# Kernel optimization log

Measured on AMD Instinct MI355X. Metric: run time of the kernel, lower is better.

The kernel has to match this reference:

```python
import jax, jax.numpy as jnp
import numpy as np

N_NODES = 4096
N_EDGES = 131072
IN_DIM = 40
HID = 128
OUT = 128
GAT_H = 2
GAT_C = 64
D_MODEL = 128
N_HEAD = 4
FF_DIM = 2048
N_LAYERS = 2
EPS = 1e-5
NEG_SLOPE = 0.2


def _layer_norm(x, g, b):
    mu = x.mean(-1, keepdims=True)
    var = ((x - mu) ** 2).mean(-1, keepdims=True)
    return (x - mu) / jnp.sqrt(var + EPS) * g + b


def _gat_conv(h, src, dst, W, a_src, a_dst, bias):
    # PyG GATConv, concat=True, eval mode (no dropout). Self loops already in (src, dst).
    N = h.shape[0]
    xw = (h @ W.T).reshape(N, GAT_H, GAT_C)          # [N, H, C]
    al_src = (xw * a_src).sum(-1)                     # [N, H]
    al_dst = (xw * a_dst).sum(-1)                     # [N, H]
    e = jax.nn.leaky_relu(al_src[src] + al_dst[dst], NEG_SLOPE)  # [E, H]
    # segment softmax over incoming edges of each dst node
    m = jax.ops.segment_max(e, dst, num_segments=N)
    ex = jnp.exp(e - m[dst])
    s = jax.ops.segment_sum(ex, dst, num_segments=N)
    alpha = ex / (s[dst] + 1e-16)                     # [E, H]
    out = jax.ops.segment_sum(xw[src] * alpha[..., None], dst, num_segments=N)
    return out.reshape(N, GAT_H * GAT_C) + bias


def _encoder_layer(x, p):
    # post-norm nn.TransformerEncoderLayer, relu FFN, eval mode
    (in_w, in_b, out_w, out_b, ln1_g, ln1_b,
     ff_w1, ff_b1, ff_w2, ff_b2, ln2_g, ln2_b) = p
    S, E = x.shape
    Dh = E // N_HEAD
    qkv = x @ in_w.T + in_b                           # [S, 3E]
    q, k, v = [t.reshape(S, N_HEAD, Dh) for t in jnp.split(qkv, 3, axis=-1)]
    scores = jnp.einsum('shd,thd->hst', q, k) / jnp.asarray(np.sqrt(Dh), x.dtype)
    attn = jax.nn.softmax(scores, axis=-1)            # [H, S, S]
    o = jnp.einsum('hst,thd->shd', attn, v).reshape(S, E) @ out_w.T + out_b
    x = _layer_norm(x + o, ln1_g, ln1_b)
    ff = jax.nn.relu(x @ ff_w1.T + ff_b1) @ ff_w2.T + ff_b2
    return _layer_norm(x + ff, ln2_g, ln2_b)


def _forward(floats, edge_index):
    (x, enc_w1, enc_b1, enc_w2, enc_b2,
     gat_w, gat_asrc, gat_adst, gat_b,
     l0_in_w, l0_in_b, l0_out_w, l0_out_b, l0_ln1_g, l0_ln1_b,
     l0_ff_w1, l0_ff_b1, l0_ff_w2, l0_ff_b2, l0_ln2_g, l0_ln2_b,
     l1_in_w, l1_in_b, l1_out_w, l1_out_b, l1_ln1_g, l1_ln1_b,
     l1_ff_w1, l1_ff_b1, l1_ff_w2, l1_ff_b2, l1_ln2_g, l1_ln2_b) = floats
    N = x.shape[0]
    # encoder MLP
    h = jax.nn.relu(x @ enc_w1.T + enc_b1) @ enc_w2.T + enc_b2
    # add one self loop per node (GATConv add_self_loops semantics)
    loop = jnp.arange(N, dtype=edge_index.dtype)
    src = jnp.concatenate([edge_index[0], loop])
    dst = jnp.concatenate([edge_index[1], loop])
    h = _gat_conv(h, src, dst, gat_w, gat_asrc, gat_adst, gat_b)
    layers = [
        (l0_in_w, l0_in_b, l0_out_w, l0_out_b, l0_ln1_g, l0_ln1_b,
         l0_ff_w1, l0_ff_b1, l0_ff_w2, l0_ff_b2, l0_ln2_g, l0_ln2_b),
        (l1_in_w, l1_in_b, l1_out_w, l1_out_b, l1_ln1_g, l1_ln1_b,
         l1_ff_w1, l1_ff_b1, l1_ff_w2, l1_ff_b2, l1_ln2_g, l1_ln2_b),
    ]
    for p in layers:
        h = _encoder_layer(h, p)
    return h


def setup_inputs() -> dict:
    key = jax.random.key(0)
    ks = jax.random.split(key, 40)
    s = 0.05
    inp = {}
    inp['x'] = jax.random.normal(ks[0], (N_NODES, IN_DIM), dtype=jnp.float32)
    # edges with src != dst (self loops added inside reference)
    src = jax.random.randint(ks[1], (N_EDGES,), 0, N_NODES)
    off = jax.random.randint(ks[2], (N_EDGES,), 1, N_NODES)
    dst = (src + off) % N_NODES
    inp['edge_index'] = jnp.stack([src, dst]).astype(jnp.int64)
    inp['enc_w1'] = jax.random.normal(ks[3], (HID, IN_DIM)) * s
    inp['enc_b1'] = jnp.zeros((HID,), jnp.float32)
    inp['enc_w2'] = jax.random.normal(ks[4], (OUT, HID)) * s
    inp['enc_b2'] = jnp.zeros((OUT,), jnp.float32)
    inp['gat_w'] = jax.random.normal(ks[5], (GAT_H * GAT_C, OUT)) * s
    inp['gat_asrc'] = jax.random.normal(ks[6], (GAT_H, GAT_C)) * s
    inp['gat_adst'] = jax.random.normal(ks[7], (GAT_H, GAT_C)) * s
    inp['gat_b'] = jnp.zeros((GAT_H * GAT_C,), jnp.float32)
    for i in range(N_LAYERS):
        k = jax.random.split(ks[8 + i], 8)
        inp[f'l{i}_in_w'] = jax.random.normal(k[0], (3 * D_MODEL, D_MODEL)) * s
        inp[f'l{i}_in_b'] = jnp.zeros((3 * D_MODEL,), jnp.float32)
        inp[f'l{i}_out_w'] = jax.random.normal(k[1], (D_MODEL, D_MODEL)) * s
        inp[f'l{i}_out_b'] = jnp.zeros((D_MODEL,), jnp.float32)
        inp[f'l{i}_ln1_g'] = jnp.ones((D_MODEL,), jnp.float32)
        inp[f'l{i}_ln1_b'] = jnp.zeros((D_MODEL,), jnp.float32)
        inp[f'l{i}_ff_w1'] = jax.random.normal(k[2], (FF_DIM, D_MODEL)) * s
        inp[f'l{i}_ff_b1'] = jnp.zeros((FF_DIM,), jnp.float32)
        inp[f'l{i}_ff_w2'] = jax.random.normal(k[3], (D_MODEL, FF_DIM)) * s
        inp[f'l{i}_ff_b2'] = jnp.zeros((D_MODEL,), jnp.float32)
        inp[f'l{i}_ln2_g'] = jnp.ones((D_MODEL,), jnp.float32)
        inp[f'l{i}_ln2_b'] = jnp.zeros((D_MODEL,), jnp.float32)
    return inp


def reference(x, edge_index, enc_w1, enc_b1, enc_w2, enc_b2,
              gat_w, gat_asrc, gat_adst, gat_b,
              l0_in_w, l0_in_b, l0_out_w, l0_out_b, l0_ln1_g, l0_ln1_b,
              l0_ff_w1, l0_ff_b1, l0_ff_w2, l0_ff_b2, l0_ln2_g, l0_ln2_b,
              l1_in_w, l1_in_b, l1_out_w, l1_out_b, l1_ln1_g, l1_ln1_b,
              l1_ff_w1, l1_ff_b1, l1_ff_w2, l1_ff_b2, l1_ln2_g, l1_ln2_b):
    floats = (x, enc_w1, enc_b1, enc_w2, enc_b2,
              gat_w, gat_asrc, gat_adst, gat_b,
              l0_in_w, l0_in_b, l0_out_w, l0_out_b, l0_ln1_g, l0_ln1_b,
              l0_ff_w1, l0_ff_b1, l0_ff_w2, l0_ff_b2, l0_ln2_g, l0_ln2_b,
              l1_in_w, l1_in_b, l1_out_w, l1_out_b, l1_ln1_g, l1_ln1_b,
              l1_ff_w1, l1_ff_b1, l1_ff_w2, l1_ff_b2, l1_ln2_g, l1_ln2_b)
    return _forward(floats, edge_index)
```

## Files before the change

kernel.cpp:

```cpp
#include <hip/hip_runtime.h>
#include <hip/hip_bf16.h>

typedef __hip_bfloat16 bf16;

#define N_NODES 4096
#define IN_DIM  40
#define DM      128
#define FF_DIM  2048
#define GAT_H   2
#define GAT_C   64
#define NHEAD   4
#define DH      32
#define LN_EPS  1e-5f
#define KSPLIT  8
#define FSPLIT  4

typedef short s8v __attribute__((ext_vector_type(8)));
typedef float f4v __attribute__((ext_vector_type(4)));

__device__ __forceinline__ float anyload(const void* p, size_t i, int isbf) {
    if (isbf) return __bfloat162float(((const bf16*)p)[i]);
    return ((const float*)p)[i];
}
__device__ __forceinline__ int geti(const int* ei, int i, int is64) {
    return is64 ? ei[2 * (size_t)i] : ei[i];
}
__device__ __forceinline__ ushort tob(float v) {
    bf16 b = __float2bfloat16(v);
    return *(ushort*)&b;
}

__global__ void probe_kernel(const void* ones_vec, const int* ei, int* flags,
                             int* __restrict__ deg) {
    int i = blockIdx.x * 256 + threadIdx.x;
    if (i < N_NODES) deg[i] = 0;
    if (i == 0) {
        unsigned u = ((const unsigned*)ones_vec)[0];
        flags[0] = (u == 0x3F803F80u) ? 1 : 0;
        const unsigned* e = (const unsigned*)ei;
        flags[1] = (e[1] == 0u && e[3] == 0u && e[5] == 0u && e[7] == 0u) ? 1 : 0;
    }
}

__global__ __launch_bounds__(256) void enc1_mfma_kernel(const void* __restrict__ X,
                                                        const void* __restrict__ W,
                                                        const void* __restrict__ bias,
                                                        ushort* __restrict__ Cb,
                                                        const int* __restrict__ flags) {
    const int isbf = flags[0];
    const int t = threadIdx.x;
    const int w = t >> 6, lane = t & 63;
    const int col = lane & 15, quad = lane >> 4;
    const int wr = (w & 1) * 16, wc = (w >> 1) * 32;
    const int row0 = blockIdx.y * 32, col0 = blockIdx.x * 64;
    __shared__ __align__(16) ushort As[32 * 72];
    __shared__ __align__(16) ushort Ws[64 * 72];
    {
        int r = t >> 3, c0 = (t & 7) * 8;
#pragma unroll
        for (int j = 0; j < 8; ++j) {
            int c = c0 + j;
            float v = (c < IN_DIM) ? anyload(X, (size_t)(row0 + r) * IN_DIM + c, isbf) : 0.f;
            As[r * 72 + c] = tob(v);
        }
    }
#pragma unroll
    for (int i = 0; i < 2; ++i) {
        int idx = t + i * 256;
        int r = idx >> 3, c0 = (idx & 7) * 8;
#pragma unroll
        for (int j = 0; j < 8; ++j) {
            int c = c0 + j;
            float v = (c < IN_DIM) ? anyload(W, (size_t)(col0 + r) * IN_DIM + c, isbf) : 0.f;
            Ws[r * 72 + c] = tob(v);
        }
    }
    __syncthreads();
    f4v zero = {0.f, 0.f, 0.f, 0.f};
    f4v acc[2] = {zero, zero};
    s8v a0  = *(const s8v*)&As[(wr + col) * 72 + quad * 8];
    s8v a1  = *(const s8v*)&As[(wr + col) * 72 + 32 + quad * 8];
    s8v b00 = *(const s8v*)&Ws[(wc + col) * 72 + quad * 8];
    s8v b10 = *(const s8v*)&Ws[(wc + 16 + col) * 72 + quad * 8];
    s8v b01 = *(const s8v*)&Ws[(wc + col) * 72 + 32 + quad * 8];
    s8v b11 = *(const s8v*)&Ws[(wc + 16 + col) * 72 + 32 + quad * 8];
    acc[0] = __builtin_amdgcn_mfma_f32_16x16x32_bf16(a0, b00, acc[0], 0, 0, 0);
    acc[1] = __builtin_amdgcn_mfma_f32_16x16x32_bf16(a0, b10, acc[1], 0, 0, 0);
    acc[0] = __builtin_amdgcn_mfma_f32_16x16x32_bf16(a1, b01, acc[0], 0, 0, 0);
    acc[1] = __builtin_amdgcn_mfma_f32_16x16x32_bf16(a1, b11, acc[1], 0, 0, 0);
#pragma unroll
    for (int nc = 0; nc < 2; ++nc) {
        int cc = col0 + wc + nc * 16 + col;
        float bv = anyload(bias, cc, isbf);
#pragma unroll
        for (int r = 0; r < 4; ++r) {
            int rr = row0 + wr + quad * 4 + r;
            float v = fmaxf(acc[nc][r] + bv, 0.f);
            Cb[(size_t)rr * DM + cc] = tob(v);
        }
    }
}

#define K128STR 136
__global__ __launch_bounds__(256) void k128_gemm_kernel(const ushort* __restrict__ A,
                                                        const float* __restrict__ pO,
                                                        const float* __restrict__ pL,
                                                        const void* __restrict__ W,
                                                        const void* __restrict__ bias,
                                                        float* __restrict__ Cf,
                                                        ushort* __restrict__ Cb,
                                                        ushort* __restrict__ vtb,
                                                        int N,
                                                        const int* __restrict__ flags,
                                                        int relu) {
    const int isbf = flags[0];
    const int t = threadIdx.x;
    const int w = t >> 6, lane = t & 63;
    const int col = lane & 15, quad = lane >> 4;
    const int wc = w * 16;
    const int row0 = blockIdx.y * 16, col0 = blockIdx.x * 64;
    __shared__ __align__(16) ushort As[16 * K128STR];
    __shared__ __align__(16) ushort Ws[64 * K128STR];

    {
        int ar = t >> 4, ac = (t & 15) * 8;
        if (pO) {
            int rr = row0 + ar;
            int hh = ac >> 5, d0 = ac & 31;
            size_t qi0 = ((size_t)rr) * NHEAD + hh;
            float lsum = 0.f;
            float osum[8] = {};
#pragma unroll
            for (int kz = 0; kz < KSPLIT; ++kz) {
                size_t qi = qi0 + (size_t)kz * N_NODES * NHEAD;
                lsum += pL[qi];
                const float* po = &pO[qi * 32 + d0];
#pragma unroll
                for (int j = 0; j < 8; ++j) osum[j] += po[j];
            }
            float inv = 1.f / lsum;
#pragma unroll
            for (int j = 0; j < 8; ++j) As[ar * K128STR + ac + j] = tob(osum[j] * inv);
        } else {
            *(uint4*)&As[ar * K128STR + ac] = *(const uint4*)&A[(size_t)(row0 + ar) * DM + ac];
        }
    }
    if (isbf) {
        const ushort* Wb = (const ushort*)W;
#pragma unroll
        for (int i = 0; i < 4; ++i) {
            int idx = t + i * 256;
            int r = idx >> 4, c = (idx & 15) * 8;
            *(uint4*)&Ws[r * K128STR + c] = *(const uint4*)&Wb[(size_t)(col0 + r) * DM + c];
        }
    } else {
        const float* Wf = (const float*)W;
#pragma unroll
        for (int i = 0; i < 4; ++i) {
            int idx = t + i * 256;
            int r = idx >> 4, c = (idx & 15) * 8;
#pragma unroll
            for (int j = 0; j < 8; ++j)
                Ws[r * K128STR + c + j] = tob(Wf[(size_t)(col0 + r) * DM + c + j]);
        }
    }
    __syncthreads();

    f4v acc = {0.f, 0.f, 0.f, 0.f};
#pragma unroll
    for (int j = 0; j < 4; ++j) {
        s8v a = *(const s8v*)&As[col * K128STR + j * 32 + quad * 8];
        s8v b = *(const s8v*)&Ws[(wc + col) * K128STR + j * 32 + quad * 8];
        acc = __builtin_amdgcn_mfma_f32_16x16x32_bf16(a, b, acc, 0, 0, 0);
    }

    int cc = col0 + wc + col;
    float bv = bias ? anyload(bias, cc, isbf) : 0.f;
#pragma unroll
    for (int r = 0; r < 4; ++r) {
        int rr = row0 + quad * 4 + r;
        float v = acc[r] + bv;
        if (relu) v = fmaxf(v, 0.f);
        size_t off = (size_t)rr * N + cc;
        if (Cf) Cf[off] = v;
        if (Cb) Cb[off] = tob(v);
        if (vtb && cc >= 256) vtb[(size_t)(cc - 256) * N_NODES + rr] = tob(v);
    }
}

__global__ __launch_bounds__(256) void mfma_gemm_splitk_kernel(const ushort* __restrict__ A,
                                                               const void* __restrict__ W,
                                                               float* __restrict__ Cpart,
                                                               int M, int N, int K, int kchunk,
                                                               const int* __restrict__ flags) {
    const int isbf = flags[0];
    const int t = threadIdx.x;
    const int w = t >> 6, lane = t & 63;
    const int col = lane & 15, quad = lane >> 4;
    const int wr = (w & 1) * 16, wc = (w >> 1) * 32;
    const int row0 = blockIdx.y * 32, col0 = blockIdx.x * 64;
    const int kz = blockIdx.z;
    const int k_beg = kz * kchunk, k_end = k_beg + kchunk;
    __shared__ __align__(16) ushort As[32 * 72];
    __shared__ __align__(16) ushort Ws[64 * 72];
    f4v zero = {0.f, 0.f, 0.f, 0.f};
    f4v acc[2] = {zero, zero};
    const int ar = t >> 3, ac = (t & 7) * 8;
    for (int k0 = k_beg; k0 < k_end; k0 += 64) {
        __syncthreads();
        *(uint4*)&As[ar * 72 + ac] = *(const uint4*)&A[(size_t)(row0 + ar) * K + k0 + ac];
        if (isbf) {
            const ushort* Wb = (const ushort*)W;
#pragma unroll
            for (int i = 0; i < 2; ++i) {
                int idx = t + i * 256;
                int r = idx >> 3, c = (idx & 7) * 8;
                *(uint4*)&Ws[r * 72 + c] = *(const uint4*)&Wb[(size_t)(col0 + r) * K + k0 + c];
            }
        } else {
            const float* Wf = (const float*)W;
#pragma unroll
            for (int i = 0; i < 2; ++i) {
                int idx = t + i * 256;
                int r = idx >> 3, c = (idx & 7) * 8;
#pragma unroll
                for (int j = 0; j < 8; ++j)
                    Ws[r * 72 + c + j] = tob(Wf[(size_t)(col0 + r) * K + k0 + c + j]);
            }
        }
        __syncthreads();
        s8v a0  = *(const s8v*)&As[(wr + col) * 72 + quad * 8];
        s8v a1  = *(const s8v*)&As[(wr + col) * 72 + 32 + quad * 8];
        s8v b00 = *(const s8v*)&Ws[(wc + col) * 72 + quad * 8];
        s8v b10 = *(const s8v*)&Ws[(wc + 16 + col) * 72 + quad * 8];
        s8v b01 = *(const s8v*)&Ws[(wc + col) * 72 + 32 + quad * 8];
        s8v b11 = *(const s8v*)&Ws[(wc + 16 + col) * 72 + 32 + quad * 8];
        acc[0] = __builtin_amdgcn_mfma_f32_16x16x32_bf16(a0, b00, acc[0], 0, 0, 0);
        acc[1] = __builtin_amdgcn_mfma_f32_16x16x32_bf16(a0, b10, acc[1], 0, 0, 0);
        acc[0] = __builtin_amdgcn_mfma_f32_16x16x32_bf16(a1, b01, acc[0], 0, 0, 0);
        acc[1] = __builtin_amdgcn_mfma_f32_16x16x32_bf16(a1, b11, acc[1], 0, 0, 0);
    }
#pragma unroll
    for (int nc = 0; nc < 2; ++nc) {
        int cc = col0 + wc + nc * 16 + col;
#pragma unroll
        for (int r = 0; r < 4; ++r) {
            int rr = row0 + wr + quad * 4 + r;
            Cpart[((size_t)kz * M + rr) * N + cc] = acc[nc][r];
        }
    }
}

__global__ void deg_hist_kernel(const int* __restrict__ ei, int E0,
                                int* __restrict__ deg, const int* __restrict__ flags) {
    const int is64 = flags[1];
    int e = blockIdx.x * 256 + threadIdx.x;
    int E = E0 + N_NODES;
    if (e >= E) return;
    int d = (e < E0) ? geti(ei, E0 + e, is64) : (e - E0);
    atomicAdd(&deg[d], 1);
}

__global__ __launch_bounds__(256) void scan_kernel(const int* __restrict__ deg,
                                                   int* __restrict__ rowptr,
                                                   int* __restrict__ cursor) {
    __shared__ int part[256];
    const int t = threadIdx.x;
    const int base = t * 16;
    int loc[16];
    int s = 0;
#pragma unroll
    for (int i = 0; i < 16; ++i) { loc[i] = s; s += deg[base + i]; }
    part[t] = s;
    __syncthreads();
    for (int d = 1; d < 256; d <<= 1) {
        int v = (t >= d) ? part[t - d] : 0;
        __syncthreads();
        part[t] += v;
        __syncthreads();
    }
    int prev = (t == 0) ? 0 : part[t - 1];
#pragma unroll
    for (int i = 0; i < 16; ++i) {
        int r = prev + loc[i];
        rowptr[base + i] = r;
        cursor[base + i] = r;
    }
    if (t == 255) rowptr[N_NODES] = part[255];
}

__global__ void scatter_kernel(const int* __restrict__ ei, int E0,
                               int* __restrict__ cursor, int* __restrict__ csr_src,
                               const int* __restrict__ flags) {
    const int is64 = flags[1];
    int e = blockIdx.x * 256 + threadIdx.x;
    int E = E0 + N_NODES;
    if (e >= E) return;
    int s = (e < E0) ? geti(ei, e, is64) : (e - E0);
    int d = (e < E0) ? geti(ei, E0 + e, is64) : (e - E0);
    int pos = atomicAdd(&cursor[d], 1);
    csr_src[pos] = s;
}

__global__ void gat_al_kernel(const float* __restrict__ xw,
                              const void* __restrict__ asrc,
                              const void* __restrict__ adst,
                              float* __restrict__ als, float* __restrict__ ald,
                              const int* __restrict__ flags) {
    const int isbf = flags[0];
    int i = blockIdx.x * 256 + threadIdx.x;
    if (i >= N_NODES * GAT_H) return;
    int n = i >> 1, h = i & 1;
    const float* xr = xw + (size_t)n * DM + h * GAT_C;
    float ss = 0.f, sd = 0.f;
#pragma unroll 4
    for (int c = 0; c < GAT_C; ++c) {
        float v = xr[c];
        ss += v * anyload(asrc, h * GAT_C + c, isbf);
        sd += v * anyload(adst, h * GAT_C + c, isbf);
    }
    als[i] = ss;
    ald[i] = sd;
}

__global__ __launch_bounds__(256) void gat_gather_kernel(const int* __restrict__ rowptr,
                                                         const int* __restrict__ csr_src,
                                                         const float* __restrict__ als,
                                                         const float* __restrict__ ald,
                                                         const float* __restrict__ xw,
                                                         const void* __restrict__ gat_b,
                                                         float* __restrict__ hg,
                                                         ushort* __restrict__ hgb,
                                                         const int* __restrict__ flags) {
    const int isbf = flags[0];
    const int idx = blockIdx.x * 4 + (threadIdx.x >> 6);
    const int lane = threadIdx.x & 63;
    const int d = idx >> 1, hh = idx & 1;
    const int beg = rowptr[d], end = rowptr[d + 1];
    const float aldv = ald[d * 2 + hh];

    float mx = -3.0e38f;
    for (int i = beg + lane; i < end; i += 64) {
        int s = csr_src[i];
        float v = als[s * 2 + hh] + aldv;
        v = (v > 0.f) ? v : 0.2f * v;
        mx = fmaxf(mx, v);
    }
#pragma unroll
    for (int o = 32; o >= 1; o >>= 1) mx = fmaxf(mx, __shfl_xor(mx, o));
    float sm = 0.f;
    for (int i = beg + lane; i < end; i += 64) {
        int s = csr_src[i];
        float v = als[s * 2 + hh] + aldv;
        v = (v > 0.f) ? v : 0.2f * v;
        sm += __expf(v - mx);
    }
#pragma unroll
    for (int o = 32; o >= 1; o >>= 1) sm += __shfl_xor(sm, o);
    const float inv = 1.f / (sm + 1e-16f);

    float o_acc = 0.f;
    for (int i = beg; i < end; ++i) {
        int s = csr_src[i];
        float v = als[s * 2 + hh] + aldv;
        v = (v > 0.f) ? v : 0.2f * v;
        float alpha = __expf(v - mx) * inv;
        o_acc += alpha * xw[(size_t)s * DM + hh * GAT_C + lane];
    }
    float outv = o_acc + anyload(gat_b, hh * GAT_C + lane, isbf);
    size_t off = (size_t)d * DM + hh * GAT_C + lane;
    hg[off] = outv;
    hgb[off] = tob(outv);
}

#define KSTR 40
#define VSTR 136
#define PSTR 136
__global__ __launch_bounds__(256) void attn_mfma_kernel(const ushort* __restrict__ qkvb,
                                                        const ushort* __restrict__ vtb,
                                                        float* __restrict__ pO,
                                                        float* __restrict__ pL) {
    const int hh = blockIdx.y;
    const int kz = blockIdx.z;
    const int t = threadIdx.x;
    const int w = t >> 6;
    const int lane = t & 63;
    const int col = lane & 15;
    const int quad = lane >> 4;
    const int qr = blockIdx.x * 64 + w * 16;

    __shared__ __align__(16) ushort Ks[128 * KSTR];
    __shared__ __align__(16) ushort Vt[32 * VSTR];
    __shared__ __align__(16) ushort Pl[4][16 * PSTR];

    s8v aq = *(const s8v*)&qkvb[(size_t)(qr + col) * 384 + hh * 32 + quad * 8];

    f4v zero = {0.f, 0.f, 0.f, 0.f};
    f4v of[2] = {zero, zero};
    float lacc[4] = {0.f, 0.f, 0.f, 0.f};
    const float scale = 0.17677669529663687f;
    const int k_beg = kz * (N_NODES / KSPLIT);
    const int k_end = k_beg + (N_NODES / KSPLIT);

    for (int kt = k_beg; kt < k_end; kt += 128) {
        __syncthreads();
        for (int idx = t; idx < 512; idx += 256) {
            int r = idx >> 2, c = (idx & 3) * 8;
            *(uint4*)&Ks[r * KSTR + c] =
                *(const uint4*)&qkvb[(size_t)(kt + r) * 384 + 128 + hh * 32 + c];
        }
        for (int idx = t; idx < 512; idx += 256) {
            int d = idx >> 4, c = (idx & 15) * 8;
            *(uint4*)&Vt[d * VSTR + c] =
                *(const uint4*)&vtb[(size_t)(hh * 32 + d) * N_NODES + kt + c];
        }
        __syncthreads();

        f4v sf[8];
#pragma unroll
        for (int kb = 0; kb < 8; ++kb) {
            s8v bk = *(const s8v*)&Ks[(kb * 16 + col) * KSTR + quad * 8];
            sf[kb] = __builtin_amdgcn_mfma_f32_16x16x32_bf16(aq, bk, zero, 0, 0, 0);
        }
#pragma unroll
        for (int kb = 0; kb < 8; ++kb) {
#pragma unroll
            for (int r = 0; r < 4; ++r) {
                float p = __expf(sf[kb][r] * scale);
                lacc[r] += p;
                Pl[w][(quad * 4 + r) * PSTR + kb * 16 + col] = tob(p);
            }
        }
#pragma unroll
        for (int kc = 0; kc < 4; ++kc) {
            s8v ap = *(const s8v*)&Pl[w][col * PSTR + kc * 32 + quad * 8];
#pragma unroll
            for (int nc = 0; nc < 2; ++nc) {
                s8v bv = *(const s8v*)&Vt[(nc * 16 + col) * VSTR + kc * 32 + quad * 8];
                of[nc] = __builtin_amdgcn_mfma_f32_16x16x32_bf16(ap, bv, of[nc], 0, 0, 0);
            }
        }
    }
#pragma unroll
    for (int r = 0; r < 4; ++r) {
        float lv = lacc[r];
#pragma unroll
        for (int off = 1; off <= 8; off <<= 1) lv += __shfl_xor(lv, off);
        int row = quad * 4 + r;
        size_t qi = ((size_t)kz * N_NODES + qr + row) * NHEAD + hh;
#pragma unroll
        for (int nc = 0; nc < 2; ++nc)
            pO[qi * 32 + nc * 16 + col] = of[nc][r];
        if (col == 0) pL[qi] = lv;
    }
}

__global__ __launch_bounds__(256) void ln_kernel(float* __restrict__ h, const float* __restrict__ y,
                                                 ushort* __restrict__ hb,
                                                 const void* __restrict__ g, const void* __restrict__ b,
                                                 const int* __restrict__ flags) {
    const int isbf = flags[0];
    const int row = blockIdx.x * 4 + (threadIdx.x >> 6);
    const int lane = threadIdx.x & 63;
    const size_t base = (size_t)row * DM;
    float v0 = h[base + lane] + y[base + lane];
    float v1 = h[base + 64 + lane] + y[base + 64 + lane];
    float s = v0 + v1;
#pragma unroll
    for (int o = 32; o >= 1; o >>= 1) s += __shfl_xor(s, o);
    float mu = s * (1.f / DM);
    float d0 = v0 - mu, d1 = v1 - mu;
    float q = d0 * d0 + d1 * d1;
#pragma unroll
    for (int o = 32; o >= 1; o >>= 1) q += __shfl_xor(q, o);
    float rstd = rsqrtf(q * (1.f / DM) + LN_EPS);
    float o0 = d0 * rstd * anyload(g, lane, isbf) + anyload(b, lane, isbf);
    float o1 = d1 * rstd * anyload(g, 64 + lane, isbf) + anyload(b, 64 + lane, isbf);
    h[base + lane] = o0;       h[base + 64 + lane] = o1;
    hb[base + lane] = tob(o0); hb[base + 64 + lane] = tob(o1);
}

__global__ __launch_bounds__(256) void ln4_kernel(float* __restrict__ h,
                                                  const float* __restrict__ pC,
                                                  const void* __restrict__ fbias,
                                                  ushort* __restrict__ hb,
                                                  const void* __restrict__ g, const void* __restrict__ b,
                                                  const int* __restrict__ flags) {
    const int isbf = flags[0];
    const int row = blockIdx.x * 4 + (threadIdx.x >> 6);
    const int lane = threadIdx.x & 63;
    const size_t base = (size_t)row * DM;
    float y0 = anyload(fbias, lane, isbf), y1 = anyload(fbias, 64 + lane, isbf);
#pragma unroll
    for (int kz = 0; kz < FSPLIT; ++kz) {
        size_t pb = (size_t)kz * N_NODES * DM + base;
        y0 += pC[pb + lane];
        y1 += pC[pb + 64 + lane];
    }
    float v0 = h[base + lane] + y0;
    float v1 = h[base + 64 + lane] + y1;
    float s = v0 + v1;
#pragma unroll
    for (int o = 32; o >= 1; o >>= 1) s += __shfl_xor(s, o);
    float mu = s * (1.f / DM);
    float d0 = v0 - mu, d1 = v1 - mu;
    float q = d0 * d0 + d1 * d1;
#pragma unroll
    for (int o = 32; o >= 1; o >>= 1) q += __shfl_xor(q, o);
    float rstd = rsqrtf(q * (1.f / DM) + LN_EPS);
    float o0 = d0 * rstd * anyload(g, lane, isbf) + anyload(b, lane, isbf);
    float o1 = d1 * rstd * anyload(g, 64 + lane, isbf) + anyload(b, 64 + lane, isbf);
    h[base + lane] = o0;       h[base + 64 + lane] = o1;
    hb[base + lane] = tob(o0); hb[base + 64 + lane] = tob(o1);
}

__global__ void convert_out_kernel(const float* __restrict__ h, void* __restrict__ out, int n,
                                   const int* __restrict__ flags) {
    const int isbf = flags[0];
    int i = blockIdx.x * 256 + threadIdx.x;
    if (i < n) {
        if (isbf) ((ushort*)out)[i] = tob(h[i]);
        else      ((float*)out)[i] = h[i];
    }
}

extern "C" void kernel_launch(void* const* d_in, const int* in_sizes, int n_in,
                              void* d_out, int out_size, void* d_ws, size_t ws_size,
                              hipStream_t stream) {
    const void* x        = d_in[0];
    const int*  ei       = (const int*)d_in[1];
    const void* enc_w1   = d_in[2];
    const void* enc_b1   = d_in[3];
    const void* enc_w2   = d_in[4];
    const void* enc_b2   = d_in[5];
    const void* gat_w    = d_in[6];
    const void* gat_asrc = d_in[7];
    const void* gat_adst = d_in[8];
    const void* gat_b    = d_in[9];
    const void *in_w[2], *in_b[2], *out_w[2], *out_b[2], *ln1_g[2], *ln1_b[2];
    const void *ff_w1[2], *ff_b1[2], *ff_w2[2], *ff_b2[2], *ln2_g[2], *ln2_b[2];
    for (int L = 0; L < 2; ++L) {
        int base = 10 + L * 12;
        in_w[L]  = d_in[base + 0];
        in_b[L]  = d_in[base + 1];
        out_w[L] = d_in[base + 2];
        out_b[L] = d_in[base + 3];
        ln1_g[L] = d_in[base + 4];
        ln1_b[L] = d_in[base + 5];
        ff_w1[L] = d_in[base + 6];
        ff_b1[L] = d_in[base + 7];
        ff_w2[L] = d_in[base + 8];
        ff_b2[L] = d_in[base + 9];
        ln2_g[L] = d_in[base + 10];
        ln2_b[L] = d_in[base + 11];
    }
    const int E0 = in_sizes[1] / 2;
    const int E  = E0 + N_NODES;
    const size_t NN = N_NODES;

    int*    flags   = (int*)d_ws;
    float*  h       = (float*)d_ws + 64;
    float*  tmp     = h + NN * DM;
    ushort* hb      = (ushort*)(tmp + NN * DM);
    ushort* hid     = hb + NN * DM;
    ushort* qkvb    = hid + NN * DM;
    ushort* vtb     = qkvb + NN * 384;
    float*  pO      = (float*)(vtb + NN * DM);
    float*  pL      = pO + (size_t)KSPLIT * NN * NHEAD * 32;
    float*  pC      = pL + (size_t)KSPLIT * NN * NHEAD;
    ushort* ff1b    = (ushort*)(pC + (size_t)FSPLIT * NN * DM);
    float*  xw      = (float*)(ff1b + NN * FF_DIM);
    float*  als     = xw + NN * DM;
    float*  ald     = als + NN * GAT_H;
    int*    deg     = (int*)(ald + NN * GAT_H);
    int*    rowptr  = deg + N_NODES;
    int*    cursor  = rowptr + N_NODES + 1;
    int*    csr_src = cursor + N_NODES;

    dim3 blk(256);

    probe_kernel<<<dim3(16), blk, 0, stream>>>(ln1_g[0], ei, flags, deg);
    deg_hist_kernel<<<dim3((E + 255) / 256), blk, 0, stream>>>(ei, E0, deg, flags);
    scan_kernel<<<dim3(1), blk, 0, stream>>>(deg, rowptr, cursor);
    scatter_kernel<<<dim3((E + 255) / 256), blk, 0, stream>>>(ei, E0, cursor, csr_src, flags);

    enc1_mfma_kernel<<<dim3(DM / 64, N_NODES / 32), blk, 0, stream>>>(
        x, enc_w1, enc_b1, hid, flags);
    k128_gemm_kernel<<<dim3(DM / 64, N_NODES / 16), blk, 0, stream>>>(
        hid, nullptr, nullptr, enc_w2, enc_b2, nullptr, hb, nullptr, DM, flags, 0);

    k128_gemm_kernel<<<dim3(DM / 64, N_NODES / 16), blk, 0, stream>>>(
        hb, nullptr, nullptr, gat_w, nullptr, xw, nullptr, nullptr, DM, flags, 0);
    gat_al_kernel<<<dim3((N_NODES * GAT_H + 255) / 256), blk, 0, stream>>>(
        xw, gat_asrc, gat_adst, als, ald, flags);
    gat_gather_kernel<<<dim3(N_NODES * GAT_H / 4), blk, 0, stream>>>(
        rowptr, csr_src, als, ald, xw, gat_b, h, hb, flags);

    for (int L = 0; L < 2; ++L) {
        k128_gemm_kernel<<<dim3(3 * DM / 64, N_NODES / 16), blk, 0, stream>>>(
            hb, nullptr, nullptr, in_w[L], in_b[L], nullptr, qkvb, vtb, 3 * DM, flags, 0);
        attn_mfma_kernel<<<dim3(N_NODES / 64, NHEAD, KSPLIT), blk, 0, stream>>>(
            qkvb, vtb, pO, pL);
        k128_gemm_kernel<<<dim3(DM / 64, N_NODES / 16), blk, 0, stream>>>(
            nullptr, pO, pL, out_w[L], out_b[L], tmp, nullptr, nullptr, DM, flags, 0);
        ln_kernel<<<dim3(N_NODES / 4), blk, 0, stream>>>(h, tmp, hb, ln1_g[L], ln1_b[L], flags);
        k128_gemm_kernel<<<dim3(FF_DIM / 64, N_NODES / 16), blk, 0, stream>>>(
            hb, nullptr, nullptr, ff_w1[L], ff_b1[L], nullptr, ff1b, nullptr, FF_DIM, flags, 1);
        mfma_gemm_splitk_kernel<<<dim3(DM / 64, N_NODES / 32, FSPLIT), blk, 0, stream>>>(
            ff1b, ff_w2[L], pC, N_NODES, DM, FF_DIM, FF_DIM / FSPLIT, flags);
        ln4_kernel<<<dim3(N_NODES / 4), blk, 0, stream>>>(h, pC, ff_b2[L], hb, ln2_g[L], ln2_b[L], flags);
    }

    convert_out_kernel<<<dim3((out_size + 255) / 256), blk, 0, stream>>>(h, d_out, out_size, flags);
}
```

Measured before the change: 357.3 us.

## Fuse encoder GEMM with GAT projection, out-proj with LayerNorm, and output conversion

Merges the second encoder GEMM, the GAT weight GEMM and the attention-logit reduction into one kernel that keeps the intermediate row tile in shared memory. Fuses the attention output projection (including split-K merge of partial outputs) with the residual add and LayerNorm, which removes the fp32 tmp buffer and a separate launch. Folds the final dtype conversion into the last LayerNorm kernel. Together these remove several launches and global round trips. The cost is fewer blocks (256 instead of 512) for the fused kernels, each loading the full 128x128 weight.

```diff
diff --git a/kernel.cpp b/kernel.cpp
--- a/kernel.cpp
+++ b/kernel.cpp
@@ -103,11 +103,8 @@
 
 #define K128STR 136
 __global__ __launch_bounds__(256) void k128_gemm_kernel(const ushort* __restrict__ A,
-                                                        const float* __restrict__ pO,
-                                                        const float* __restrict__ pL,
                                                         const void* __restrict__ W,
                                                         const void* __restrict__ bias,
-                                                        float* __restrict__ Cf,
                                                         ushort* __restrict__ Cb,
                                                         ushort* __restrict__ vtb,
                                                         int N,
@@ -121,29 +118,9 @@
     const int row0 = blockIdx.y * 16, col0 = blockIdx.x * 64;
     __shared__ __align__(16) ushort As[16 * K128STR];
     __shared__ __align__(16) ushort Ws[64 * K128STR];
-
     {
         int ar = t >> 4, ac = (t & 15) * 8;
-        if (pO) {
-            int rr = row0 + ar;
-            int hh = ac >> 5, d0 = ac & 31;
-            size_t qi0 = ((size_t)rr) * NHEAD + hh;
-            float lsum = 0.f;
-            float osum[8] = {};
-#pragma unroll
-            for (int kz = 0; kz < KSPLIT; ++kz) {
-                size_t qi = qi0 + (size_t)kz * N_NODES * NHEAD;
-                lsum += pL[qi];
-                const float* po = &pO[qi * 32 + d0];
-#pragma unroll
-                for (int j = 0; j < 8; ++j) osum[j] += po[j];
-            }
-            float inv = 1.f / lsum;
-#pragma unroll
-            for (int j = 0; j < 8; ++j) As[ar * K128STR + ac + j] = tob(osum[j] * inv);
-        } else {
-            *(uint4*)&As[ar * K128STR + ac] = *(const uint4*)&A[(size_t)(row0 + ar) * DM + ac];
-        }
+        *(uint4*)&As[ar * K128STR + ac] = *(const uint4*)&A[(size_t)(row0 + ar) * DM + ac];
     }
     if (isbf) {
         const ushort* Wb = (const ushort*)W;
@@ -165,7 +142,6 @@
         }
     }
     __syncthreads();
-
     f4v acc = {0.f, 0.f, 0.f, 0.f};
 #pragma unroll
     for (int j = 0; j < 4; ++j) {
@@ -173,7 +149,6 @@
         s8v b = *(const s8v*)&Ws[(wc + col) * K128STR + j * 32 + quad * 8];
         acc = __builtin_amdgcn_mfma_f32_16x16x32_bf16(a, b, acc, 0, 0, 0);
     }
-
     int cc = col0 + wc + col;
     float bv = bias ? anyload(bias, cc, isbf) : 0.f;
 #pragma unroll
@@ -181,10 +156,236 @@
         int rr = row0 + quad * 4 + r;
         float v = acc[r] + bv;
         if (relu) v = fmaxf(v, 0.f);
-        size_t off = (size_t)rr * N + cc;
-        if (Cf) Cf[off] = v;
-        if (Cb) Cb[off] = tob(v);
+        Cb[(size_t)rr * N + cc] = tob(v);
         if (vtb && cc >= 256) vtb[(size_t)(cc - 256) * N_NODES + rr] = tob(v);
+    }
+}
+
+__global__ __launch_bounds__(256) void enc2_gat_kernel(const ushort* __restrict__ hid,
+                                                       const void* __restrict__ w2,
+                                                       const void* __restrict__ b2,
+                                                       const void* __restrict__ gw,
+                                                       const void* __restrict__ asrc,
+                                                       const void* __restrict__ adst,
+                                                       ushort* __restrict__ hb,
+                                                       float* __restrict__ xw,
+                                                       float* __restrict__ als,
+                                                       float* __restrict__ ald,
+                                                       const int* __restrict__ flags) {
+    const int isbf = flags[0];
+    const int t = threadIdx.x;
+    const int w = t >> 6, lane = t & 63;
+    const int col = lane & 15, quad = lane >> 4;
+    const int row0 = blockIdx.x * 16;
+    __shared__ __align__(16) ushort As[16 * K128STR];
+    __shared__ __align__(16) ushort Ws[128 * K128STR];
+    __shared__ float Cs[16][132];
+
+    {
+        int ar = t >> 4, ac = (t & 15) * 8;
+        *(uint4*)&As[ar * K128STR + ac] = *(const uint4*)&hid[(size_t)(row0 + ar) * DM + ac];
+    }
+    if (isbf) {
+        const ushort* Wb = (const ushort*)w2;
+#pragma unroll
+        for (int i = 0; i < 8; ++i) {
+            int idx = t + i * 256;
+            int r = idx >> 4, c = (idx & 15) * 8;
+            *(uint4*)&Ws[r * K128STR + c] = *(const uint4*)&Wb[(size_t)r * DM + c];
+        }
+    } else {
+        const float* Wf = (const float*)w2;
+#pragma unroll
+        for (int i = 0; i < 8; ++i) {
+            int idx = t + i * 256;
+            int r = idx >> 4, c = (idx & 15) * 8;
+#pragma unroll
+            for (int j = 0; j < 8; ++j)
+                Ws[r * K128STR + c + j] = tob(Wf[(size_t)r * DM + c + j]);
+        }
+    }
+    __syncthreads();
+    f4v zero = {0.f, 0.f, 0.f, 0.f};
+    f4v acc[2] = {zero, zero};
+#pragma unroll
+    for (int nc = 0; nc < 2; ++nc)
+#pragma unroll
+        for (int j = 0; j < 4; ++j) {
+            s8v a = *(const s8v*)&As[col * K128STR + j * 32 + quad * 8];
+            s8v b = *(const s8v*)&Ws[(w * 32 + nc * 16 + col) * K128STR + j * 32 + quad * 8];
+            acc[nc] = __builtin_amdgcn_mfma_f32_16x16x32_bf16(a, b, acc[nc], 0, 0, 0);
+        }
+    __syncthreads();
+#pragma unroll
+    for (int nc = 0; nc < 2; ++nc) {
+        int cc = w * 32 + nc * 16 + col;
+        float bv = anyload(b2, cc, isbf);
+#pragma unroll
+        for (int r = 0; r < 4; ++r) {
+            int row = quad * 4 + r;
+            float v = acc[nc][r] + bv;
+            ushort hv = tob(v);
+            hb[(size_t)(row0 + row) * DM + cc] = hv;
+            As[row * K128STR + cc] = hv;
+        }
+    }
+    if (isbf) {
+        const ushort* Wb = (const ushort*)gw;
+#pragma unroll
+        for (int i = 0; i < 8; ++i) {
+            int idx = t + i * 256;
+            int r = idx >> 4, c = (idx & 15) * 8;
+            *(uint4*)&Ws[r * K128STR + c] = *(const uint4*)&Wb[(size_t)r * DM + c];
+        }
+    } else {
+        const float* Wf = (const float*)gw;
+#pragma unroll
+        for (int i = 0; i < 8; ++i) {
+            int idx = t + i * 256;
+            int r = idx >> 4, c = (idx & 15) * 8;
+#pragma unroll
+            for (int j = 0; j < 8; ++j)
+                Ws[r * K128STR + c + j] = tob(Wf[(size_t)r * DM + c + j]);
+        }
+    }
+    __syncthreads();
+    f4v acc2[2] = {zero, zero};
+#pragma unroll
+    for (int nc = 0; nc < 2; ++nc)
+#pragma unroll
+        for (int j = 0; j < 4; ++j) {
+            s8v a = *(const s8v*)&As[col * K128STR + j * 32 + quad * 8];
+            s8v b = *(const s8v*)&Ws[(w * 32 + nc * 16 + col) * K128STR + j * 32 + quad * 8];
+            acc2[nc] = __builtin_amdgcn_mfma_f32_16x16x32_bf16(a, b, acc2[nc], 0, 0, 0);
+        }
+#pragma unroll
+    for (int nc = 0; nc < 2; ++nc) {
+        int cc = w * 32 + nc * 16 + col;
+#pragma unroll
+        for (int r = 0; r < 4; ++r) {
+            int row = quad * 4 + r;
+            float v = acc2[nc][r];
+            xw[(size_t)(row0 + row) * DM + cc] = v;
+            Cs[row][cc] = v;
+        }
+    }
+    __syncthreads();
+#pragma unroll
+    for (int rr = 0; rr < 4; ++rr) {
+        int row = w * 4 + rr;
+        float x0 = Cs[row][lane], x1 = Cs[row][64 + lane];
+        float s0 = x0 * anyload(asrc, lane, isbf);
+        float d0 = x0 * anyload(adst, lane, isbf);
+        float s1 = x1 * anyload(asrc, 64 + lane, isbf);
+        float d1 = x1 * anyload(adst, 64 + lane, isbf);
+#pragma unroll
+        for (int o = 32; o >= 1; o >>= 1) {
+            s0 += __shfl_xor(s0, o); d0 += __shfl_xor(d0, o);
+            s1 += __shfl_xor(s1, o); d1 += __shfl_xor(d1, o);
+        }
+        if (lane == 0) {
+            int n = row0 + row;
+            als[n * 2 + 0] = s0; ald[n * 2 + 0] = d0;
+            als[n * 2 + 1] = s1; ald[n * 2 + 1] = d1;
+        }
+    }
+}
+
+__global__ __launch_bounds__(256) void oproj_ln_kernel(const float* __restrict__ pO,
+                                                       const float* __restrict__ pL,
+                                                       const void* __restrict__ W,
+                                                       const void* __restrict__ bias,
+                                                       float* __restrict__ h,
+                                                       ushort* __restrict__ hb,
+                                                       const void* __restrict__ g,
+                                                       const void* __restrict__ b,
+                                                       const int* __restrict__ flags) {
+    const int isbf = flags[0];
+    const int t = threadIdx.x;
+    const int w = t >> 6, lane = t & 63;
+    const int col = lane & 15, quad = lane >> 4;
+    const int row0 = blockIdx.x * 16;
+    __shared__ __align__(16) ushort As[16 * K128STR];
+    __shared__ __align__(16) ushort Ws[128 * K128STR];
+    __shared__ float Cs[16][132];
+
+    {
+        int ar = t >> 4, ac = (t & 15) * 8;
+        int rr = row0 + ar;
+        int hh = ac >> 5, d0 = ac & 31;
+        size_t qi0 = ((size_t)rr) * NHEAD + hh;
+        float lsum = 0.f;
+        float osum[8] = {};
+#pragma unroll
+        for (int kz = 0; kz < KSPLIT; ++kz) {
+            size_t qi = qi0 + (size_t)kz * N_NODES * NHEAD;
+            lsum += pL[qi];
+            const float* po = &pO[qi * 32 + d0];
+#pragma unroll
+            for (int j = 0; j < 8; ++j) osum[j] += po[j];
+        }
+        float inv = 1.f / lsum;
+#pragma unroll
+        for (int j = 0; j < 8; ++j) As[ar * K128STR + ac + j] = tob(osum[j] * inv);
+    }
+    if (isbf) {
+        const ushort* Wb = (const ushort*)W;
+#pragma unroll
+        for (int i = 0; i < 8; ++i) {
+            int idx = t + i * 256;
+            int r = idx >> 4, c = (idx & 15) * 8;
+            *(uint4*)&Ws[r * K128STR + c] = *(const uint4*)&Wb[(size_t)r * DM + c];
+        }
+    } else {
+        const float* Wf = (const float*)W;
+#pragma unroll
+        for (int i = 0; i < 8; ++i) {
+            int idx = t + i * 256;
+            int r = idx >> 4, c = (idx & 15) * 8;
+#pragma unroll
+            for (int j = 0; j < 8; ++j)
+                Ws[r * K128STR + c + j] = tob(Wf[(size_t)r * DM + c + j]);
+        }
+    }
+    __syncthreads();
+    f4v zero = {0.f, 0.f, 0.f, 0.f};
+    f4v acc[2] = {zero, zero};
+#pragma unroll
+    for (int nc = 0; nc < 2; ++nc)
+#pragma unroll
+        for (int j = 0; j < 4; ++j) {
+            s8v a = *(const s8v*)&As[col * K128STR + j * 32 + quad * 8];
+            s8v b = *(const s8v*)&Ws[(w * 32 + nc * 16 + col) * K128STR + j * 32 + quad * 8];
+            acc[nc] = __builtin_amdgcn_mfma_f32_16x16x32_bf16(a, b, acc[nc], 0, 0, 0);
+        }
+#pragma unroll
+    for (int nc = 0; nc < 2; ++nc) {
+        int cc = w * 32 + nc * 16 + col;
+        float bv = bias ? anyload(bias, cc, isbf) : 0.f;
+#pragma unroll
+        for (int r = 0; r < 4; ++r)
+            Cs[quad * 4 + r][cc] = acc[nc][r] + bv;
+    }
+    __syncthreads();
+#pragma unroll
+    for (int rr = 0; rr < 4; ++rr) {
+        int row = w * 4 + rr;
+        size_t base = (size_t)(row0 + row) * DM;
+        float v0 = h[base + lane] + Cs[row][lane];
+        float v1 = h[base + 64 + lane] + Cs[row][64 + lane];
+        float s = v0 + v1;
+#pragma unroll
+        for (int o = 32; o >= 1; o >>= 1) s += __shfl_xor(s, o);
+        float mu = s * (1.f / DM);
+        float d0 = v0 - mu, d1 = v1 - mu;
+        float q = d0 * d0 + d1 * d1;
+#pragma unroll
+        for (int o = 32; o >= 1; o >>= 1) q += __shfl_xor(q, o);
+        float rstd = rsqrtf(q * (1.f / DM) + LN_EPS);
+        float o0 = d0 * rstd * anyload(g, lane, isbf) + anyload(b, lane, isbf);
+        float o1 = d1 * rstd * anyload(g, 64 + lane, isbf) + anyload(b, 64 + lane, isbf);
+        h[base + lane] = o0;       h[base + 64 + lane] = o1;
+        hb[base + lane] = tob(o0); hb[base + 64 + lane] = tob(o1);
     }
 }
 
@@ -302,27 +503,6 @@
     csr_src[pos] = s;
 }
 
-__global__ void gat_al_kernel(const float* __restrict__ xw,
-                              const void* __restrict__ asrc,
-                              const void* __restrict__ adst,
-                              float* __restrict__ als, float* __restrict__ ald,
-                              const int* __restrict__ flags) {
-    const int isbf = flags[0];
-    int i = blockIdx.x * 256 + threadIdx.x;
-    if (i >= N_NODES * GAT_H) return;
-    int n = i >> 1, h = i & 1;
-    const float* xr = xw + (size_t)n * DM + h * GAT_C;
-    float ss = 0.f, sd = 0.f;
-#pragma unroll 4
-    for (int c = 0; c < GAT_C; ++c) {
-        float v = xr[c];
-        ss += v * anyload(asrc, h * GAT_C + c, isbf);
-        sd += v * anyload(adst, h * GAT_C + c, isbf);
-    }
-    als[i] = ss;
-    ald[i] = sd;
-}
-
 __global__ __launch_bounds__(256) void gat_gather_kernel(const int* __restrict__ rowptr,
                                                          const int* __restrict__ csr_src,
                                                          const float* __restrict__ als,
@@ -455,16 +635,26 @@
     }
 }
 
-__global__ __launch_bounds__(256) void ln_kernel(float* __restrict__ h, const float* __restrict__ y,
-                                                 ushort* __restrict__ hb,
-                                                 const void* __restrict__ g, const void* __restrict__ b,
-                                                 const int* __restrict__ flags) {
+__global__ __launch_bounds__(256) void ln4_kernel(float* __restrict__ h,
+                                                  const float* __restrict__ pC,
+                                                  const void* __restrict__ fbias,
+                                                  ushort* __restrict__ hb,
+                                                  const void* __restrict__ g, const void* __restrict__ b,
+                                                  void* __restrict__ outp,
+                                                  const int* __restrict__ flags) {
     const int isbf = flags[0];
     const int row = blockIdx.x * 4 + (threadIdx.x >> 6);
     const int lane = threadIdx.x & 63;
     const size_t base = (size_t)row * DM;
-    float v0 = h[base + lane] + y[base + lane];
-    float v1 = h[base + 64 + lane] + y[base + 64 + lane];
+    float y0 = anyload(fbias, lane, isbf), y1 = anyload(fbias, 64 + lane, isbf);
+#pragma unroll
+    for (int kz = 0; kz < FSPLIT; ++kz) {
+        size_t pb = (size_t)kz * N_NODES * DM + base;
+        y0 += pC[pb + lane];
+        y1 += pC[pb + 64 + lane];
+    }
+    float v0 = h[base + lane] + y0;
+    float v1 = h[base + 64 + lane] + y1;
     float s = v0 + v1;
 #pragma unroll
     for (int o = 32; o >= 1; o >>= 1) s += __shfl_xor(s, o);
@@ -478,49 +668,14 @@
     float o1 = d1 * rstd * anyload(g, 64 + lane, isbf) + anyload(b, 64 + lane, isbf);
     h[base + lane] = o0;       h[base + 64 + lane] = o1;
     hb[base + lane] = tob(o0); hb[base + 64 + lane] = tob(o1);
-}
-
-__global__ __launch_bounds__(256) void ln4_kernel(float* __restrict__ h,
-                                                  const float* __restrict__ pC,
-                                                  const void* __restrict__ fbias,
-                                                  ushort* __restrict__ hb,
-                                                  const void* __restrict__ g, const void* __restrict__ b,
-                                                  const int* __restrict__ flags) {
-    const int isbf = flags[0];
-    const int row = blockIdx.x * 4 + (threadIdx.x >> 6);
-    const int lane = threadIdx.x & 63;
-    const size_t base = (size_t)row * DM;
-    float y0 = anyload(fbias, lane, isbf), y1 = anyload(fbias, 64 + lane, isbf);
-#pragma unroll
-    for (int kz = 0; kz < FSPLIT; ++kz) {
-        size_t pb = (size_t)kz * N_NODES * DM + base;
-        y0 += pC[pb + lane];
-        y1 += pC[pb + 64 + lane];
-    }
-    float v0 = h[base + lane] + y0;
-    float v1 = h[base + 64 + lane] + y1;
-    float s = v0 + v1;
-#pragma unroll
-    for (int o = 32; o >= 1; o >>= 1) s += __shfl_xor(s, o);
-    float mu = s * (1.f / DM);
-    float d0 = v0 - mu, d1 = v1 - mu;
-    float q = d0 * d0 + d1 * d1;
-#pragma unroll
-    for (int o = 32; o >= 1; o >>= 1) q += __shfl_xor(q, o);
-    float rstd = rsqrtf(q * (1.f / DM) + LN_EPS);
-    float o0 = d0 * rstd * anyload(g, lane, isbf) + anyload(b, lane, isbf);
-    float o1 = d1 * rstd * anyload(g, 64 + lane, isbf) + anyload(b, 64 + lane, isbf);
-    h[base + lane] = o0;       h[base + 64 + lane] = o1;
-    hb[base + lane] = tob(o0); hb[base + 64 + lane] = tob(o1);
-}
-
-__global__ void convert_out_kernel(const float* __restrict__ h, void* __restrict__ out, int n,
-                                   const int* __restrict__ flags) {
-    const int isbf = flags[0];
-    int i = blockIdx.x * 256 + threadIdx.x;
-    if (i < n) {
-        if (isbf) ((ushort*)out)[i] = tob(h[i]);
-        else      ((float*)out)[i] = h[i];
+    if (outp) {
+        if (isbf) {
+            ((ushort*)outp)[base + lane] = tob(o0);
+            ((ushort*)outp)[base + 64 + lane] = tob(o1);
+        } else {
+            ((float*)outp)[base + lane] = o0;
+            ((float*)outp)[base + 64 + lane] = o1;
+        }
     }
 }
 
@@ -560,8 +715,7 @@
 
     int*    flags   = (int*)d_ws;
     float*  h       = (float*)d_ws + 64;
-    float*  tmp     = h + NN * DM;
-    ushort* hb      = (ushort*)(tmp + NN * DM);
+    ushort* hb      = (ushort*)(h + NN * DM);
     ushort* hid     = hb + NN * DM;
     ushort* qkvb    = hid + NN * DM;
     ushort* vtb     = qkvb + NN * 384;
@@ -586,30 +740,24 @@
 
     enc1_mfma_kernel<<<dim3(DM / 64, N_NODES / 32), blk, 0, stream>>>(
         x, enc_w1, enc_b1, hid, flags);
-    k128_gemm_kernel<<<dim3(DM / 64, N_NODES / 16), blk, 0, stream>>>(
-        hid, nullptr, nullptr, enc_w2, enc_b2, nullptr, hb, nullptr, DM, flags, 0);
-
-    k128_gemm_kernel<<<dim3(DM / 64, N_NODES / 16), blk, 0, stream>>>(
-        hb, nullptr, nullptr, gat_w, nullptr, xw, nullptr, nullptr, DM, flags, 0);
-    gat_al_kernel<<<dim3((N_NODES * GAT_H + 255) / 256), blk, 0, stream>>>(
-        xw, gat_asrc, gat_adst, als, ald, flags);
+    enc2_gat_kernel<<<dim3(N_NODES / 16), blk, 0, stream>>>(
+        hid, enc_w2, enc_b2, gat_w, gat_asrc, gat_adst, hb, xw, als, ald, flags);
     gat_gather_kernel<<<dim3(N_NODES * GAT_H / 4), blk, 0, stream>>>(
         rowptr, csr_src, als, ald, xw, gat_b, h, hb, flags);
 
     for (int L = 0; L < 2; ++L) {
         k128_gemm_kernel<<<dim3(3 * DM / 64, N_NODES / 16), blk, 0, stream>>>(
-            hb, nullptr, nullptr, in_w[L], in_b[L], nullptr, qkvb, vtb, 3 * DM, flags, 0);
+            hb, in_w[L], in_b[L], qkvb, vtb, 3 * DM, flags, 0);
         attn_mfma_kernel<<<dim3(N_NODES / 64, NHEAD, KSPLIT), blk, 0, stream>>>(
             qkvb, vtb, pO, pL);
-        k128_gemm_kernel<<<dim3(DM / 64, N_NODES / 16), blk, 0, stream>>>(
-            nullptr, pO, pL, out_w[L], out_b[L], tmp, nullptr, nullptr, DM, flags, 0);
-        ln_kernel<<<dim3(N_NODES / 4), blk, 0, stream>>>(h, tmp, hb, ln1_g[L], ln1_b[L], flags);
+        oproj_ln_kernel<<<dim3(N_NODES / 16), blk, 0, stream>>>(
+            pO, pL, out_w[L], out_b[L], h, hb, ln1_g[L], ln1_b[L], flags);
         k128_gemm_kernel<<<dim3(FF_DIM / 64, N_NODES / 16), blk, 0, stream>>>(
-            hb, nullptr, nullptr, ff_w1[L], ff_b1[L], nullptr, ff1b, nullptr, FF_DIM, flags, 1);
+            hb, ff_w1[L], ff_b1[L], ff1b, nullptr, FF_DIM, flags, 1);
         mfma_gemm_splitk_kernel<<<dim3(DM / 64, N_NODES / 32, FSPLIT), blk, 0, stream>>>(
             ff1b, ff_w2[L], pC, N_NODES, DM, FF_DIM, FF_DIM / FSPLIT, flags);
-        ln4_kernel<<<dim3(N_NODES / 4), blk, 0, stream>>>(h, pC, ff_b2[L], hb, ln2_g[L], ln2_b[L], flags);
-    }
-
-    convert_out_kernel<<<dim3((out_size + 255) / 256), blk, 0, stream>>>(h, d_out, out_size, flags);
-}
+        ln4_kernel<<<dim3(N_NODES / 4), blk, 0, stream>>>(
+            h, pC, ff_b2[L], hb, ln2_g[L], ln2_b[L],
+            (L == 1) ? d_out : nullptr, flags);
+    }
+}
```

After: 341.5 us (median of 3 runs). 4.4% less time.
